# Kernel tuning notes

Hardware: AMD Instinct MI355X
Metric: run time of the kernel (lower is better)

Reference implementation:

```python
import jax, jax.numpy as jnp
import numpy as np

N_NODES = 50000
N_EDGES = 1600000
IN_FEAT = 256
HIDDEN = 128
N_CLASSES = 16


def gcn_conv(x, edge_index, W, b, n_nodes):
    """PyG GCNConv: x' = D^{-1/2} (A+I) D^{-1/2} (x @ W) + b."""
    h = x @ W  # project first (PyG order), messages are in out_dim
    src, dst = edge_index[0], edge_index[1]
    loops = jnp.arange(n_nodes, dtype=src.dtype)
    src = jnp.concatenate([src, loops])
    dst = jnp.concatenate([dst, loops])
    # degree of A+I (count incoming edges incl. self loop)
    deg = jax.ops.segment_sum(jnp.ones_like(dst, dtype=h.dtype), dst, num_segments=n_nodes)
    dis = jax.lax.rsqrt(deg)  # deg >= 1 thanks to self loops
    norm = dis[src] * dis[dst]  # [E+N]
    msgs = h[src] * norm[:, None]  # gather + scale
    out = jax.ops.segment_sum(msgs, dst, num_segments=n_nodes)  # scatter-add
    return out + b


def setup_inputs() -> dict:
    key = jax.random.key(0)
    k_x, k_e, k_w1, k_b1, k_w2, k_b2 = jax.random.split(key, 6)
    x = jax.random.normal(k_x, (N_NODES, IN_FEAT), dtype=jnp.float32)
    edge_index = jax.random.randint(k_e, (2, N_EDGES), 0, N_NODES, dtype=jnp.int64)
    s1 = 1.0 / np.sqrt(IN_FEAT)
    s2 = 1.0 / np.sqrt(HIDDEN)
    W1 = jax.random.uniform(k_w1, (IN_FEAT, HIDDEN), jnp.float32, -s1, s1)
    b1 = jax.random.uniform(k_b1, (HIDDEN,), jnp.float32, -s1, s1)
    W2 = jax.random.uniform(k_w2, (HIDDEN, N_CLASSES), jnp.float32, -s2, s2)
    b2 = jax.random.uniform(k_b2, (N_CLASSES,), jnp.float32, -s2, s2)
    return {"x": x, "edge_index": edge_index, "W1": W1, "b1": b1, "W2": W2, "b2": b2}


def reference(x, edge_index, W1, b1, W2, b2):
    n = x.shape[0]
    h = gcn_conv(x, edge_index, W1, b1, n)
    h = jax.nn.relu(h)
    logits = gcn_conv(h, edge_index, W2, b2, n)
    return logits, jax.nn.softmax(logits, axis=1)
```

## Files before the change

### kernel.cpp

```cpp
#include <hip/hip_runtime.h>
#include <hip/hip_bf16.h>
#include <math.h>

#define N_NODES 50000
#define N_EDGES 1600000
#define IN_FEAT 256
#define HIDDEN 128
#define N_CLASSES 16

#define ECHUNK 8192
#define NCHK 196
#define NBKT 196
#define BCAP 10240

typedef __attribute__((ext_vector_type(8))) short short8;
typedef __attribute__((ext_vector_type(4))) float floatx4;

__device__ __forceinline__ unsigned short f2bf(float f) {
    unsigned u = __float_as_uint(f);
    return (unsigned short)((u + 0x7fffu + ((u >> 16) & 1u)) >> 16);
}

__device__ __forceinline__ unsigned pk2bf(float a, float b) {
    __hip_bfloat162 h = __float22bfloat162_rn(make_float2(a, b));
    union { __hip_bfloat162 h; unsigned u; } cv;
    cv.h = h;
    return cv.u;
}

__device__ __forceinline__ float bflo(unsigned u) { return __uint_as_float(u << 16); }
__device__ __forceinline__ float bfhi(unsigned u) { return __uint_as_float(u & 0xffff0000u); }

__global__ __launch_bounds__(256) void scatter_edges2(const int* __restrict__ src,
                                                      const int* __restrict__ dst,
                                                      int* __restrict__ cursor,
                                                      unsigned int* __restrict__ sorted,
                                                      const float* __restrict__ W1,
                                                      unsigned short* __restrict__ w1t) {
    __shared__ int hloc[256];
    int t = threadIdx.x;
    hloc[t] = 0;
    if (blockIdx.x < HIDDEN)
        w1t[blockIdx.x * IN_FEAT + t] = f2bf(W1[t * HIDDEN + blockIdx.x]);
    __syncthreads();
    int base = blockIdx.x * ECHUNK;
    int end = min(base + ECHUNK, N_EDGES);
    for (int i = base + t; i < end; i += 256)
        atomicAdd(&hloc[dst[i] >> 8], 1);
    __syncthreads();
    int cnt = hloc[t];
    int lbase = t * BCAP + atomicAdd(&cursor[t], cnt);
    __syncthreads();
    hloc[t] = lbase;
    __syncthreads();
    for (int i = base + t; i < end; i += 256) {
        int d = dst[i];
        int s = src[i];
        int pos = atomicAdd(&hloc[d >> 8], 1);
        sorted[pos] = ((unsigned)d << 16) | (unsigned)s;
    }
}

__global__ __launch_bounds__(256) void build_csr2(const unsigned int* __restrict__ sorted,
                                                  const int* __restrict__ cursor,
                                                  int* __restrict__ rs,
                                                  int* __restrict__ re,
                                                  float* __restrict__ dis,
                                                  unsigned short* __restrict__ csr_src) {
    __shared__ int cnt[256];
    __shared__ int roff[256];
    int t = threadIdx.x;
    int bkt = blockIdx.x;
    int ebase = bkt * BCAP;
    int eend = ebase + cursor[bkt];
    cnt[t] = 0;
    __syncthreads();
    for (int i = ebase + t; i < eend; i += 256)
        atomicAdd(&cnt[(sorted[i] >> 16) & 255], 1);
    __syncthreads();
    int v = cnt[t];
    roff[t] = v;
    __syncthreads();
    for (int off = 1; off < 256; off <<= 1) {
        int x = (t >= off) ? roff[t - off] : 0;
        __syncthreads();
        roff[t] += x;
        __syncthreads();
    }
    int excl = roff[t] - v;
    int node = bkt * 256 + t;
    if (node < N_NODES) {
        rs[node] = ebase + excl;
        re[node] = ebase + excl + v;
        dis[node] = 1.0f / sqrtf((float)(v + 1));
    }
    __syncthreads();
    cnt[t] = ebase + excl;
    __syncthreads();
    for (int i = ebase + t; i < eend; i += 256) {
        unsigned e = sorted[i];
        int pos = atomicAdd(&cnt[(e >> 16) & 255], 1);
        csr_src[pos] = (unsigned short)(e & 0xffffu);
    }
}

#define XCH 260

__global__ __launch_bounds__(256) void gemm1_mfma(const float* __restrict__ x,
                                                  const unsigned short* __restrict__ w1t,
                                                  const float* __restrict__ dis,
                                                  unsigned int* __restrict__ g1) {
    __shared__ float xs[2][8 * XCH];
    int tid = threadIdx.x;
    int w = tid >> 6;
    int lane = tid & 63;
    int quad = lane >> 4;
    int c = lane & 15;
    int row_base = blockIdx.x * 64;
    int wrow = (w >> 1) * 32;
    int col_base = (w & 1) * 64;

    int st_row = min(row_base + 16 * w + (lane >> 3), N_NODES - 1);
    int st_row2 = min(row_base + 16 * w + 8 + (lane >> 3), N_NODES - 1);
    const float* gp1 = x + (size_t)st_row * IN_FEAT + (lane & 7) * 4;
    const float* gp2 = x + (size_t)st_row2 * IN_FEAT + (lane & 7) * 4;

    floatx4 acc[2][4] = {};
    const unsigned short* bp[4];
#pragma unroll
    for (int nt = 0; nt < 4; ++nt)
        bp[nt] = w1t + (size_t)(col_base + nt * 16 + c) * IN_FEAT + quad * 8;

    int dwoff[2];
#pragma unroll
    for (int rt = 0; rt < 2; ++rt) {
        int rit = wrow + rt * 16 + c;
        dwoff[rt] = (rit >> 3) * XCH + (rit & 7) * 32 + quad * 8;
    }

#define STAGE(buf, k0)                                                                  \
    do {                                                                                \
        __builtin_amdgcn_global_load_lds(                                               \
            (const __attribute__((address_space(1))) void*)(gp1 + (k0)),                \
            (__attribute__((address_space(3))) void*)&xs[buf][(2 * w) * XCH], 16, 0, 0);\
        __builtin_amdgcn_global_load_lds(                                               \
            (const __attribute__((address_space(1))) void*)(gp2 + (k0)),                \
            (__attribute__((address_space(3))) void*)&xs[buf][(2 * w + 1) * XCH], 16, 0, 0);\
    } while (0)

    STAGE(0, 0);
    __syncthreads();

    int buf = 0;
#pragma unroll
    for (int kk = 0; kk < 8; ++kk) {
        if (kk < 7) STAGE(buf ^ 1, (kk + 1) * 32);
        short8 b[4];
#pragma unroll
        for (int nt = 0; nt < 4; ++nt)
            b[nt] = *(const short8*)(bp[nt] + kk * 32);
        short8 a[2];
#pragma unroll
        for (int rt = 0; rt < 2; ++rt) {
            float4 f0 = *(const float4*)&xs[buf][dwoff[rt]];
            float4 f1 = *(const float4*)&xs[buf][dwoff[rt] + 4];
            union { short8 s; unsigned u[4]; } au;
            au.u[0] = pk2bf(f0.x, f0.y);
            au.u[1] = pk2bf(f0.z, f0.w);
            au.u[2] = pk2bf(f1.x, f1.y);
            au.u[3] = pk2bf(f1.z, f1.w);
            a[rt] = au.s;
        }
#pragma unroll
        for (int rt = 0; rt < 2; ++rt)
#pragma unroll
            for (int nt = 0; nt < 4; ++nt)
                acc[rt][nt] = __builtin_amdgcn_mfma_f32_16x16x32_bf16(a[rt], b[nt], acc[rt][nt], 0, 0, 0);
        __syncthreads();
        buf ^= 1;
    }
#undef STAGE

    bool evenlane = (lane & 1) == 0;
#pragma unroll
    for (int rt = 0; rt < 2; ++rt) {
#pragma unroll
        for (int reg = 0; reg < 4; ++reg) {
            int row = row_base + wrow + rt * 16 + quad * 4 + reg;
            float dv = dis[min(row, N_NODES - 1)];
#pragma unroll
            for (int nt = 0; nt < 4; ++nt) {
                float v = acc[rt][nt][reg] * dv;
                float vo = __shfl_xor(v, 1);
                if (evenlane && row < N_NODES) {
                    unsigned pkd = (unsigned)f2bf(v) | ((unsigned)f2bf(vo) << 16);
                    int col = col_base + nt * 16 + c;
                    g1[(size_t)(col >> 5) * (N_NODES * 16) + (size_t)row * 16 + ((col & 31) >> 1)] = pkd;
                }
            }
        }
    }
}

__global__ __launch_bounds__(256) void agg1_sliced(const uint2* __restrict__ g1,
                                                   const int* __restrict__ rs,
                                                   const int* __restrict__ re,
                                                   const unsigned short* __restrict__ csr_src,
                                                   const float* __restrict__ dis,
                                                   const float* __restrict__ b1,
                                                   const float* __restrict__ W2,
                                                   float* __restrict__ g2p) {
    __shared__ float w2s[32 * 16];
    __shared__ float rbuf[4][8][36];
    int tid = threadIdx.x;
    int bi = blockIdx.x;
    int bucket = bi >> 4;
    int xcd = bi & 7;
    int slice = xcd >> 1;
    int quarter = ((bi >> 3) & 1) * 2 + (xcd & 1);

    for (int i = tid; i < 512; i += 256) w2s[i] = W2[slice * 512 + i];
    __syncthreads();

    int wave = tid >> 6, lane = tid & 63;
    int g = lane >> 3, m = lane & 7;
    const uint2* plane = g1 + (size_t)slice * (N_NODES * 8);
    float* gp = g2p + (size_t)slice * ((size_t)N_NODES * 16);
    int nbase = bucket * 256 + quarter * 64 + (wave * 8 + g) * 2;

#pragma unroll 1
    for (int nn = 0; nn < 2; ++nn) {
        int node = nbase + nn;
        if (node >= N_NODES) continue;
        uint2 su = plane[(size_t)node * 8 + m];
        float s0 = bflo(su.x), s1 = bfhi(su.x), s2 = bflo(su.y), s3 = bfhi(su.y);
        int e = rs[node], e1v = re[node];
        for (; e + 8 <= e1v; e += 8) {
            int i0 = csr_src[e + 0], i1 = csr_src[e + 1];
            int i2 = csr_src[e + 2], i3 = csr_src[e + 3];
            int i4 = csr_src[e + 4], i5 = csr_src[e + 5];
            int i6 = csr_src[e + 6], i7 = csr_src[e + 7];
            uint2 u0 = plane[(size_t)i0 * 8 + m];
            uint2 u1 = plane[(size_t)i1 * 8 + m];
            uint2 u2 = plane[(size_t)i2 * 8 + m];
            uint2 u3 = plane[(size_t)i3 * 8 + m];
            uint2 u4 = plane[(size_t)i4 * 8 + m];
            uint2 u5 = plane[(size_t)i5 * 8 + m];
            uint2 u6 = plane[(size_t)i6 * 8 + m];
            uint2 u7 = plane[(size_t)i7 * 8 + m];
            s0 += bflo(u0.x); s1 += bfhi(u0.x); s2 += bflo(u0.y); s3 += bfhi(u0.y);
            s0 += bflo(u1.x); s1 += bfhi(u1.x); s2 += bflo(u1.y); s3 += bfhi(u1.y);
            s0 += bflo(u2.x); s1 += bfhi(u2.x); s2 += bflo(u2.y); s3 += bfhi(u2.y);
            s0 += bflo(u3.x); s1 += bfhi(u3.x); s2 += bflo(u3.y); s3 += bfhi(u3.y);
            s0 += bflo(u4.x); s1 += bfhi(u4.x); s2 += bflo(u4.y); s3 += bfhi(u4.y);
            s0 += bflo(u5.x); s1 += bfhi(u5.x); s2 += bflo(u5.y); s3 += bfhi(u5.y);
            s0 += bflo(u6.x); s1 += bfhi(u6.x); s2 += bflo(u6.y); s3 += bfhi(u6.y);
            s0 += bflo(u7.x); s1 += bfhi(u7.x); s2 += bflo(u7.y); s3 += bfhi(u7.y);
        }
        if (e < e1v) {
            int last = e1v - 1;
            int i0 = csr_src[e];
            int i1 = csr_src[min(e + 1, last)];
            int i2 = csr_src[min(e + 2, last)];
            int i3 = csr_src[min(e + 3, last)];
            int i4 = csr_src[min(e + 4, last)];
            int i5 = csr_src[min(e + 5, last)];
            int i6 = csr_src[min(e + 6, last)];
            uint2 u0 = plane[(size_t)i0 * 8 + m];
            uint2 u1 = plane[(size_t)i1 * 8 + m];
            uint2 u2 = plane[(size_t)i2 * 8 + m];
            uint2 u3 = plane[(size_t)i3 * 8 + m];
            uint2 u4 = plane[(size_t)i4 * 8 + m];
            uint2 u5 = plane[(size_t)i5 * 8 + m];
            uint2 u6 = plane[(size_t)i6 * 8 + m];
            s0 += bflo(u0.x); s1 += bfhi(u0.x); s2 += bflo(u0.y); s3 += bfhi(u0.y);
            if (e + 1 < e1v) { s0 += bflo(u1.x); s1 += bfhi(u1.x); s2 += bflo(u1.y); s3 += bfhi(u1.y); }
            if (e + 2 < e1v) { s0 += bflo(u2.x); s1 += bfhi(u2.x); s2 += bflo(u2.y); s3 += bfhi(u2.y); }
            if (e + 3 < e1v) { s0 += bflo(u3.x); s1 += bfhi(u3.x); s2 += bflo(u3.y); s3 += bfhi(u3.y); }
            if (e + 4 < e1v) { s0 += bflo(u4.x); s1 += bfhi(u4.x); s2 += bflo(u4.y); s3 += bfhi(u4.y); }
            if (e + 5 < e1v) { s0 += bflo(u5.x); s1 += bfhi(u5.x); s2 += bflo(u5.y); s3 += bfhi(u5.y); }
            if (e + 6 < e1v) { s0 += bflo(u6.x); s1 += bfhi(u6.x); s2 += bflo(u6.y); s3 += bfhi(u6.y); }
        }
        float dv = dis[node];
        float4 bb = *(const float4*)&b1[slice * 32 + 4 * m];
        float4 r;
        r.x = fmaxf(fmaf(dv, s0, bb.x), 0.f);
        r.y = fmaxf(fmaf(dv, s1, bb.y), 0.f);
        r.z = fmaxf(fmaf(dv, s2, bb.z), 0.f);
        r.w = fmaxf(fmaf(dv, s3, bb.w), 0.f);
        *(float4*)&rbuf[wave][g][4 * m] = r;
        __builtin_amdgcn_sched_barrier(0);
        float p0 = 0.f, p1 = 0.f;
#pragma unroll
        for (int f = 0; f < 32; ++f) {
            float rv = rbuf[wave][g][f];
            p0 = fmaf(rv, w2s[f * 16 + 2 * m], p0);
            p1 = fmaf(rv, w2s[f * 16 + 2 * m + 1], p1);
        }
        __builtin_amdgcn_sched_barrier(0);
        *(float2*)&gp[(size_t)node * 16 + 2 * m] = make_float2(p0, p1);
    }
}

__global__ __launch_bounds__(256) void g2_reduce(float* __restrict__ g2p,
                                                 const float* __restrict__ dis) {
    int i = blockIdx.x * 256 + threadIdx.x;
    if (i >= N_NODES * 4) return;
    const size_t PS = (size_t)N_NODES * 16 / 4;
    const float4* p = (const float4*)g2p;
    float4 a = p[i];
    float4 b = p[i + PS];
    float4 c = p[i + 2 * PS];
    float4 d = p[i + 3 * PS];
    float dv = dis[i >> 2];
    float4 r;
    r.x = dv * ((a.x + b.x) + (c.x + d.x));
    r.y = dv * ((a.y + b.y) + (c.y + d.y));
    r.z = dv * ((a.z + b.z) + (c.z + d.z));
    r.w = dv * ((a.w + b.w) + (c.w + d.w));
    ((float4*)g2p)[i] = r;
}

__global__ __launch_bounds__(256) void agg2_softmax(const float* __restrict__ g2,
                                                    const int* __restrict__ rs,
                                                    const int* __restrict__ re,
                                                    const unsigned short* __restrict__ csr_src,
                                                    const float* __restrict__ dis,
                                                    const float* __restrict__ b2,
                                                    float* __restrict__ out) {
    int tid = threadIdx.x;
    int node = blockIdx.x * 16 + (tid >> 4);
    int c = tid & 15;
    float acc0 = g2[(size_t)node * N_CLASSES + c];
    float acc1 = 0.f, acc2 = 0.f, acc3 = 0.f;
    float acc4 = 0.f, acc5 = 0.f, acc6 = 0.f, acc7 = 0.f;
    int e0 = rs[node], e1 = re[node];
    int e = e0;
    for (; e + 8 <= e1; e += 8) {
        int s0 = csr_src[e + 0], s1 = csr_src[e + 1], s2 = csr_src[e + 2], s3 = csr_src[e + 3];
        int s4 = csr_src[e + 4], s5 = csr_src[e + 5], s6 = csr_src[e + 6], s7 = csr_src[e + 7];
        acc0 += g2[(size_t)s0 * N_CLASSES + c];
        acc1 += g2[(size_t)s1 * N_CLASSES + c];
        acc2 += g2[(size_t)s2 * N_CLASSES + c];
        acc3 += g2[(size_t)s3 * N_CLASSES + c];
        acc4 += g2[(size_t)s4 * N_CLASSES + c];
        acc5 += g2[(size_t)s5 * N_CLASSES + c];
        acc6 += g2[(size_t)s6 * N_CLASSES + c];
        acc7 += g2[(size_t)s7 * N_CLASSES + c];
    }
    for (; e < e1; ++e) {
        int s = csr_src[e];
        acc0 += g2[(size_t)s * N_CLASSES + c];
    }
    acc0 = ((acc0 + acc1) + (acc2 + acc3)) + ((acc4 + acc5) + (acc6 + acc7));
    float logit = fmaf(dis[node], acc0, b2[c]);
    out[(size_t)node * N_CLASSES + c] = logit;
    float m = logit;
    for (int off = 8; off; off >>= 1) m = fmaxf(m, __shfl_xor(m, off));
    float ex = expf(logit - m);
    float s = ex;
    for (int off = 8; off; off >>= 1) s += __shfl_xor(s, off);
    out[(size_t)N_NODES * N_CLASSES + (size_t)node * N_CLASSES + c] = ex / s;
}


extern "C" void kernel_launch(void* const* d_in, const int* in_sizes, int n_in,
                              void* d_out, int out_size, void* d_ws, size_t ws_size,
                              hipStream_t stream) {
    const float* x  = (const float*)d_in[0];
    const int*   ei = (const int*)d_in[1];
    const float* W1 = (const float*)d_in[2];
    const float* b1 = (const float*)d_in[3];
    const float* W2 = (const float*)d_in[4];
    const float* b2 = (const float*)d_in[5];
    float* out = (float*)d_out;

    char* ws = (char*)d_ws;
    size_t off = 0;
    auto alloc = [&](size_t bytes) -> char* {
        char* p = ws + off;
        off = (off + bytes + 511) & ~(size_t)511;
        return p;
    };
    int*   cursor   = (int*)alloc(256 * 4);
    float* dis      = (float*)alloc(N_NODES * 4);
    int*   rs       = (int*)alloc(N_NODES * 4);
    int*   re       = (int*)alloc(N_NODES * 4);
    unsigned short* w1t = (unsigned short*)alloc((size_t)HIDDEN * IN_FEAT * 2);
    unsigned short* csr_src = (unsigned short*)alloc((size_t)NBKT * BCAP * 2);
    unsigned int* g1 = (unsigned int*)alloc((size_t)N_NODES * 64 * 4);
    float* g2p      = (float*)alloc(4 * (size_t)N_NODES * N_CLASSES * 4);
    unsigned int* sorted = (unsigned int*)g1;
    (void)ws_size; (void)in_sizes; (void)n_in; (void)out_size;

    const int* src = ei;
    const int* dst = ei + N_EDGES;

    hipMemsetAsync(cursor, 0, 256 * 4, stream);
    scatter_edges2<<<NCHK, 256, 0, stream>>>(src, dst, cursor, sorted, W1, w1t);
    build_csr2<<<NBKT, 256, 0, stream>>>(sorted, cursor, rs, re, dis, csr_src);

    gemm1_mfma<<<(N_NODES + 63) / 64, 256, 0, stream>>>(x, w1t, dis, g1);
    agg1_sliced<<<NBKT * 16, 256, 0, stream>>>((const uint2*)g1, rs, re, csr_src, dis, b1, W2, g2p);
    g2_reduce<<<(N_NODES * 4 + 255) / 256, 256, 0, stream>>>(g2p, dis);
    agg2_softmax<<<N_NODES / 16, 256, 0, stream>>>(g2p, rs, re, csr_src, dis, b2, out);
}
```

Baseline: 235.3 us.

## Widen gather loads to 16 bytes with shuffled indices and double-buffered neighbor loads

Both aggregation kernels now have each node handled by 4 lanes that load 16-byte vectors (uint4/float4), where before 8 or 16 lanes loaded narrower words. Neighbor indices are loaded cooperatively and broadcast with shuffles, and the row gathers are double-buffered with sched barriers so the next batch is in flight while the current one is accumulated. This is meant to cut the number of load instructions and index loads per edge and to hide gather latency. In exchange each lane uses more registers, which may lower occupancy, and the softmax reduction changes shape.

```diff
diff --git a/kernel.cpp b/kernel.cpp
--- a/kernel.cpp
+++ b/kernel.cpp
@@ -202,7 +202,7 @@
     }
 }
 
-__global__ __launch_bounds__(256) void agg1_sliced(const uint2* __restrict__ g1,
+__global__ __launch_bounds__(256) void agg1_sliced(const uint4* __restrict__ g1,
                                                    const int* __restrict__ rs,
                                                    const int* __restrict__ re,
                                                    const unsigned short* __restrict__ csr_src,
@@ -211,7 +211,7 @@
                                                    const float* __restrict__ W2,
                                                    float* __restrict__ g2p) {
     __shared__ float w2s[32 * 16];
-    __shared__ float rbuf[4][8][36];
+    __shared__ float rbuf[4][16][36];
     int tid = threadIdx.x;
     int bi = blockIdx.x;
     int bucket = bi >> 4;
@@ -223,83 +223,109 @@
     __syncthreads();
 
     int wave = tid >> 6, lane = tid & 63;
-    int g = lane >> 3, m = lane & 7;
-    const uint2* plane = g1 + (size_t)slice * (N_NODES * 8);
+    int g = lane >> 2, m4 = lane & 3;
+    int qb = lane & ~3;
+    const uint4* plane = g1 + (size_t)slice * (N_NODES * 4);
     float* gp = g2p + (size_t)slice * ((size_t)N_NODES * 16);
-    int nbase = bucket * 256 + quarter * 64 + (wave * 8 + g) * 2;
-
-#pragma unroll 1
-    for (int nn = 0; nn < 2; ++nn) {
-        int node = nbase + nn;
-        if (node >= N_NODES) continue;
-        uint2 su = plane[(size_t)node * 8 + m];
-        float s0 = bflo(su.x), s1 = bfhi(su.x), s2 = bflo(su.y), s3 = bfhi(su.y);
+    int node = bucket * 256 + quarter * 64 + wave * 16 + g;
+    bool alive = (node < N_NODES);
+
+#define ACC8(u) do { a0 += bflo((u).x); a1 += bfhi((u).x); a2 += bflo((u).y); a3 += bfhi((u).y); \
+                     a4 += bflo((u).z); a5 += bfhi((u).z); a6 += bflo((u).w); a7 += bfhi((u).w); } while (0)
+#define LDB(ii, U0, U1, U2, U3) do {                        \
+        int j0 = __shfl((ii), qb + 0);                      \
+        int j1 = __shfl((ii), qb + 1);                      \
+        int j2 = __shfl((ii), qb + 2);                      \
+        int j3 = __shfl((ii), qb + 3);                      \
+        U0 = plane[(size_t)j0 * 4 + m4];                    \
+        U1 = plane[(size_t)j1 * 4 + m4];                    \
+        U2 = plane[(size_t)j2 * 4 + m4];                    \
+        U3 = plane[(size_t)j3 * 4 + m4];                    \
+    } while (0)
+
+    if (alive) {
+        uint4 su = plane[(size_t)node * 4 + m4];
+        float a0 = bflo(su.x), a1 = bfhi(su.x), a2 = bflo(su.y), a3 = bfhi(su.y);
+        float a4 = bflo(su.z), a5 = bfhi(su.z), a6 = bflo(su.w), a7 = bfhi(su.w);
         int e = rs[node], e1v = re[node];
-        for (; e + 8 <= e1v; e += 8) {
-            int i0 = csr_src[e + 0], i1 = csr_src[e + 1];
-            int i2 = csr_src[e + 2], i3 = csr_src[e + 3];
-            int i4 = csr_src[e + 4], i5 = csr_src[e + 5];
-            int i6 = csr_src[e + 6], i7 = csr_src[e + 7];
-            uint2 u0 = plane[(size_t)i0 * 8 + m];
-            uint2 u1 = plane[(size_t)i1 * 8 + m];
-            uint2 u2 = plane[(size_t)i2 * 8 + m];
-            uint2 u3 = plane[(size_t)i3 * 8 + m];
-            uint2 u4 = plane[(size_t)i4 * 8 + m];
-            uint2 u5 = plane[(size_t)i5 * 8 + m];
-            uint2 u6 = plane[(size_t)i6 * 8 + m];
-            uint2 u7 = plane[(size_t)i7 * 8 + m];
-            s0 += bflo(u0.x); s1 += bfhi(u0.x); s2 += bflo(u0.y); s3 += bfhi(u0.y);
-            s0 += bflo(u1.x); s1 += bfhi(u1.x); s2 += bflo(u1.y); s3 += bfhi(u1.y);
-            s0 += bflo(u2.x); s1 += bfhi(u2.x); s2 += bflo(u2.y); s3 += bfhi(u2.y);
-            s0 += bflo(u3.x); s1 += bfhi(u3.x); s2 += bflo(u3.y); s3 += bfhi(u3.y);
-            s0 += bflo(u4.x); s1 += bfhi(u4.x); s2 += bflo(u4.y); s3 += bfhi(u4.y);
-            s0 += bflo(u5.x); s1 += bfhi(u5.x); s2 += bflo(u5.y); s3 += bfhi(u5.y);
-            s0 += bflo(u6.x); s1 += bfhi(u6.x); s2 += bflo(u6.y); s3 += bfhi(u6.y);
-            s0 += bflo(u7.x); s1 += bfhi(u7.x); s2 += bflo(u7.y); s3 += bfhi(u7.y);
-        }
-        if (e < e1v) {
-            int last = e1v - 1;
-            int i0 = csr_src[e];
-            int i1 = csr_src[min(e + 1, last)];
-            int i2 = csr_src[min(e + 2, last)];
-            int i3 = csr_src[min(e + 3, last)];
-            int i4 = csr_src[min(e + 4, last)];
-            int i5 = csr_src[min(e + 5, last)];
-            int i6 = csr_src[min(e + 6, last)];
-            uint2 u0 = plane[(size_t)i0 * 8 + m];
-            uint2 u1 = plane[(size_t)i1 * 8 + m];
-            uint2 u2 = plane[(size_t)i2 * 8 + m];
-            uint2 u3 = plane[(size_t)i3 * 8 + m];
-            uint2 u4 = plane[(size_t)i4 * 8 + m];
-            uint2 u5 = plane[(size_t)i5 * 8 + m];
-            uint2 u6 = plane[(size_t)i6 * 8 + m];
-            s0 += bflo(u0.x); s1 += bfhi(u0.x); s2 += bflo(u0.y); s3 += bfhi(u0.y);
-            if (e + 1 < e1v) { s0 += bflo(u1.x); s1 += bfhi(u1.x); s2 += bflo(u1.y); s3 += bfhi(u1.y); }
-            if (e + 2 < e1v) { s0 += bflo(u2.x); s1 += bfhi(u2.x); s2 += bflo(u2.y); s3 += bfhi(u2.y); }
-            if (e + 3 < e1v) { s0 += bflo(u3.x); s1 += bfhi(u3.x); s2 += bflo(u3.y); s3 += bfhi(u3.y); }
-            if (e + 4 < e1v) { s0 += bflo(u4.x); s1 += bfhi(u4.x); s2 += bflo(u4.y); s3 += bfhi(u4.y); }
-            if (e + 5 < e1v) { s0 += bflo(u5.x); s1 += bfhi(u5.x); s2 += bflo(u5.y); s3 += bfhi(u5.y); }
-            if (e + 6 < e1v) { s0 += bflo(u6.x); s1 += bfhi(u6.x); s2 += bflo(u6.y); s3 += bfhi(u6.y); }
-        }
+        int rem = e1v - e;
+
+        if (rem >= 4) {
+            uint4 A0, A1, A2, A3, B0, B1, B2, B3;
+            int iC = csr_src[e + m4];
+            int iN = csr_src[e + 4 + m4];
+            LDB(iC, A0, A1, A2, A3);
+            e += 4; rem -= 4;
+            while (rem >= 8) {
+                iC = iN;
+                iN = csr_src[e + 4 + m4];
+                LDB(iC, B0, B1, B2, B3);
+                __builtin_amdgcn_sched_barrier(0);
+                ACC8(A0); ACC8(A1); ACC8(A2); ACC8(A3);
+                iC = iN;
+                iN = csr_src[e + 8 + m4];
+                LDB(iC, A0, A1, A2, A3);
+                __builtin_amdgcn_sched_barrier(0);
+                ACC8(B0); ACC8(B1); ACC8(B2); ACC8(B3);
+                e += 8; rem -= 8;
+            }
+            if (rem >= 4) {
+                iC = iN;
+                LDB(iC, B0, B1, B2, B3);
+                __builtin_amdgcn_sched_barrier(0);
+                ACC8(A0); ACC8(A1); ACC8(A2); ACC8(A3);
+                ACC8(B0); ACC8(B1); ACC8(B2); ACC8(B3);
+                e += 4; rem -= 4;
+            } else {
+                ACC8(A0); ACC8(A1); ACC8(A2); ACC8(A3);
+            }
+        }
+        while (rem > 0) {
+            int j = csr_src[e];
+            uint4 u = plane[(size_t)j * 4 + m4];
+            ACC8(u);
+            ++e; --rem;
+        }
+
         float dv = dis[node];
-        float4 bb = *(const float4*)&b1[slice * 32 + 4 * m];
-        float4 r;
-        r.x = fmaxf(fmaf(dv, s0, bb.x), 0.f);
-        r.y = fmaxf(fmaf(dv, s1, bb.y), 0.f);
-        r.z = fmaxf(fmaf(dv, s2, bb.z), 0.f);
-        r.w = fmaxf(fmaf(dv, s3, bb.w), 0.f);
-        *(float4*)&rbuf[wave][g][4 * m] = r;
-        __builtin_amdgcn_sched_barrier(0);
-        float p0 = 0.f, p1 = 0.f;
-#pragma unroll
-        for (int f = 0; f < 32; ++f) {
-            float rv = rbuf[wave][g][f];
-            p0 = fmaf(rv, w2s[f * 16 + 2 * m], p0);
-            p1 = fmaf(rv, w2s[f * 16 + 2 * m + 1], p1);
-        }
-        __builtin_amdgcn_sched_barrier(0);
-        *(float2*)&gp[(size_t)node * 16 + 2 * m] = make_float2(p0, p1);
-    }
+        float4 bb0 = *(const float4*)&b1[slice * 32 + 8 * m4];
+        float4 bb1 = *(const float4*)&b1[slice * 32 + 8 * m4 + 4];
+        float4 r0, r1;
+        r0.x = fmaxf(fmaf(dv, a0, bb0.x), 0.f);
+        r0.y = fmaxf(fmaf(dv, a1, bb0.y), 0.f);
+        r0.z = fmaxf(fmaf(dv, a2, bb0.z), 0.f);
+        r0.w = fmaxf(fmaf(dv, a3, bb0.w), 0.f);
+        r1.x = fmaxf(fmaf(dv, a4, bb1.x), 0.f);
+        r1.y = fmaxf(fmaf(dv, a5, bb1.y), 0.f);
+        r1.z = fmaxf(fmaf(dv, a6, bb1.z), 0.f);
+        r1.w = fmaxf(fmaf(dv, a7, bb1.w), 0.f);
+        *(float4*)&rbuf[wave][g][8 * m4] = r0;
+        *(float4*)&rbuf[wave][g][8 * m4 + 4] = r1;
+    }
+    __builtin_amdgcn_sched_barrier(0);
+    if (alive) {
+        float p0 = 0.f, p1 = 0.f, p2 = 0.f, p3 = 0.f;
+#pragma unroll
+        for (int fb = 0; fb < 8; ++fb) {
+            float4 rv = *(const float4*)&rbuf[wave][g][fb * 4];
+            float4 w0 = *(const float4*)&w2s[(fb * 4 + 0) * 16 + 4 * m4];
+            float4 w1 = *(const float4*)&w2s[(fb * 4 + 1) * 16 + 4 * m4];
+            float4 w2 = *(const float4*)&w2s[(fb * 4 + 2) * 16 + 4 * m4];
+            float4 w3 = *(const float4*)&w2s[(fb * 4 + 3) * 16 + 4 * m4];
+            p0 = fmaf(rv.x, w0.x, p0); p1 = fmaf(rv.x, w0.y, p1);
+            p2 = fmaf(rv.x, w0.z, p2); p3 = fmaf(rv.x, w0.w, p3);
+            p0 = fmaf(rv.y, w1.x, p0); p1 = fmaf(rv.y, w1.y, p1);
+            p2 = fmaf(rv.y, w1.z, p2); p3 = fmaf(rv.y, w1.w, p3);
+            p0 = fmaf(rv.z, w2.x, p0); p1 = fmaf(rv.z, w2.y, p1);
+            p2 = fmaf(rv.z, w2.z, p2); p3 = fmaf(rv.z, w2.w, p3);
+            p0 = fmaf(rv.w, w3.x, p0); p1 = fmaf(rv.w, w3.y, p1);
+            p2 = fmaf(rv.w, w3.z, p2); p3 = fmaf(rv.w, w3.w, p3);
+        }
+        float4 pv; pv.x = p0; pv.y = p1; pv.z = p2; pv.w = p3;
+        *(float4*)&gp[(size_t)node * 16 + 4 * m4] = pv;
+    }
+#undef LDB
+#undef ACC8
 }
 
 __global__ __launch_bounds__(256) void g2_reduce(float* __restrict__ g2p,
@@ -321,7 +347,7 @@
     ((float4*)g2p)[i] = r;
 }
 
-__global__ __launch_bounds__(256) void agg2_softmax(const float* __restrict__ g2,
+__global__ __launch_bounds__(256) void agg2_softmax(const float4* __restrict__ g2,
                                                     const int* __restrict__ rs,
                                                     const int* __restrict__ re,
                                                     const unsigned short* __restrict__ csr_src,
@@ -329,38 +355,88 @@
                                                     const float* __restrict__ b2,
                                                     float* __restrict__ out) {
     int tid = threadIdx.x;
-    int node = blockIdx.x * 16 + (tid >> 4);
-    int c = tid & 15;
-    float acc0 = g2[(size_t)node * N_CLASSES + c];
-    float acc1 = 0.f, acc2 = 0.f, acc3 = 0.f;
-    float acc4 = 0.f, acc5 = 0.f, acc6 = 0.f, acc7 = 0.f;
-    int e0 = rs[node], e1 = re[node];
-    int e = e0;
-    for (; e + 8 <= e1; e += 8) {
-        int s0 = csr_src[e + 0], s1 = csr_src[e + 1], s2 = csr_src[e + 2], s3 = csr_src[e + 3];
-        int s4 = csr_src[e + 4], s5 = csr_src[e + 5], s6 = csr_src[e + 6], s7 = csr_src[e + 7];
-        acc0 += g2[(size_t)s0 * N_CLASSES + c];
-        acc1 += g2[(size_t)s1 * N_CLASSES + c];
-        acc2 += g2[(size_t)s2 * N_CLASSES + c];
-        acc3 += g2[(size_t)s3 * N_CLASSES + c];
-        acc4 += g2[(size_t)s4 * N_CLASSES + c];
-        acc5 += g2[(size_t)s5 * N_CLASSES + c];
-        acc6 += g2[(size_t)s6 * N_CLASSES + c];
-        acc7 += g2[(size_t)s7 * N_CLASSES + c];
-    }
-    for (; e < e1; ++e) {
-        int s = csr_src[e];
-        acc0 += g2[(size_t)s * N_CLASSES + c];
-    }
-    acc0 = ((acc0 + acc1) + (acc2 + acc3)) + ((acc4 + acc5) + (acc6 + acc7));
-    float logit = fmaf(dis[node], acc0, b2[c]);
-    out[(size_t)node * N_CLASSES + c] = logit;
-    float m = logit;
-    for (int off = 8; off; off >>= 1) m = fmaxf(m, __shfl_xor(m, off));
-    float ex = expf(logit - m);
-    float s = ex;
-    for (int off = 8; off; off >>= 1) s += __shfl_xor(s, off);
-    out[(size_t)N_NODES * N_CLASSES + (size_t)node * N_CLASSES + c] = ex / s;
+    int wave = tid >> 6, lane = tid & 63;
+    int g = lane >> 2, m4 = lane & 3;
+    int qb = lane & ~3;
+    int node = blockIdx.x * 64 + wave * 16 + g;
+    if (node >= N_NODES) return;
+
+    float4 acc = g2[(size_t)node * 4 + m4];
+
+#define ACC4(u) do { acc.x += (u).x; acc.y += (u).y; acc.z += (u).z; acc.w += (u).w; } while (0)
+#define LDB4(ii, U0, U1, U2, U3) do {                       \
+        int j0 = __shfl((ii), qb + 0);                      \
+        int j1 = __shfl((ii), qb + 1);                      \
+        int j2 = __shfl((ii), qb + 2);                      \
+        int j3 = __shfl((ii), qb + 3);                      \
+        U0 = g2[(size_t)j0 * 4 + m4];                       \
+        U1 = g2[(size_t)j1 * 4 + m4];                       \
+        U2 = g2[(size_t)j2 * 4 + m4];                       \
+        U3 = g2[(size_t)j3 * 4 + m4];                       \
+    } while (0)
+
+    int e = rs[node], e1v = re[node];
+    int rem = e1v - e;
+    if (rem >= 4) {
+        float4 A0, A1, A2, A3, B0, B1, B2, B3;
+        int iC = csr_src[e + m4];
+        int iN = csr_src[e + 4 + m4];
+        LDB4(iC, A0, A1, A2, A3);
+        e += 4; rem -= 4;
+        while (rem >= 8) {
+            iC = iN;
+            iN = csr_src[e + 4 + m4];
+            LDB4(iC, B0, B1, B2, B3);
+            __builtin_amdgcn_sched_barrier(0);
+            ACC4(A0); ACC4(A1); ACC4(A2); ACC4(A3);
+            iC = iN;
+            iN = csr_src[e + 8 + m4];
+            LDB4(iC, A0, A1, A2, A3);
+            __builtin_amdgcn_sched_barrier(0);
+            ACC4(B0); ACC4(B1); ACC4(B2); ACC4(B3);
+            e += 8; rem -= 8;
+        }
+        if (rem >= 4) {
+            iC = iN;
+            LDB4(iC, B0, B1, B2, B3);
+            __builtin_amdgcn_sched_barrier(0);
+            ACC4(A0); ACC4(A1); ACC4(A2); ACC4(A3);
+            ACC4(B0); ACC4(B1); ACC4(B2); ACC4(B3);
+            e += 4; rem -= 4;
+        } else {
+            ACC4(A0); ACC4(A1); ACC4(A2); ACC4(A3);
+        }
+    }
+    while (rem > 0) {
+        int j = csr_src[e];
+        float4 u = g2[(size_t)j * 4 + m4];
+        ACC4(u);
+        ++e; --rem;
+    }
+#undef LDB4
+#undef ACC4
+
+    float dv = dis[node];
+    float4 bb = *(const float4*)&b2[4 * m4];
+    float4 lg;
+    lg.x = fmaf(dv, acc.x, bb.x);
+    lg.y = fmaf(dv, acc.y, bb.y);
+    lg.z = fmaf(dv, acc.z, bb.z);
+    lg.w = fmaf(dv, acc.w, bb.w);
+    ((float4*)out)[(size_t)node * 4 + m4] = lg;
+
+    float m = fmaxf(fmaxf(lg.x, lg.y), fmaxf(lg.z, lg.w));
+    m = fmaxf(m, __shfl_xor(m, 1));
+    m = fmaxf(m, __shfl_xor(m, 2));
+    float4 ex;
+    ex.x = expf(lg.x - m); ex.y = expf(lg.y - m);
+    ex.z = expf(lg.z - m); ex.w = expf(lg.w - m);
+    float s = (ex.x + ex.y) + (ex.z + ex.w);
+    s += __shfl_xor(s, 1);
+    s += __shfl_xor(s, 2);
+    float inv = 1.0f / s;
+    ex.x *= inv; ex.y *= inv; ex.z *= inv; ex.w *= inv;
+    ((float4*)out)[(size_t)N_NODES * 4 + (size_t)node * 4 + m4] = ex;
 }
 
 
@@ -401,7 +477,7 @@
     build_csr2<<<NBKT, 256, 0, stream>>>(sorted, cursor, rs, re, dis, csr_src);
 
     gemm1_mfma<<<(N_NODES + 63) / 64, 256, 0, stream>>>(x, w1t, dis, g1);
-    agg1_sliced<<<NBKT * 16, 256, 0, stream>>>((const uint2*)g1, rs, re, csr_src, dis, b1, W2, g2p);
+    agg1_sliced<<<NBKT * 16, 256, 0, stream>>>((const uint4*)g1, rs, re, csr_src, dis, b1, W2, g2p);
     g2_reduce<<<(N_NODES * 4 + 255) / 256, 256, 0, stream>>>(g2p, dis);
-    agg2_softmax<<<N_NODES / 16, 256, 0, stream>>>(g2p, rs, re, csr_src, dis, b2, out);
-}
+    agg2_softmax<<<N_NODES / 64 + 1, 256, 0, stream>>>((const float4*)g2p, rs, re, csr_src, dis, b2, out);
+}
```

Result: faster. 223.0 us (-5.3%).
